# Kernel tuning notes

Hardware: AMD Instinct MI355X
Metric: run time of the kernel (lower is better)

Reference implementation:

```python
import jax, jax.numpy as jnp
import numpy as np

N_INNER = 2000  # number of inner tree nodes, divisible by 5 (gen_A grouping)
N_LEAF = 10000  # vocabulary / leaf count
N_DOC = 128     # number of documents


def _build_inv_A(n_inner):
    """Static structural matrix: A_full = I - [0 | A], inverted once (host-side numpy)."""
    m = n_inner // 5
    A = np.zeros((n_inner, n_inner - 1), dtype=np.float32)
    for r in range(m - 1):
        A[r, 5 * r:5 * r + 5] = 1.0
    A[m - 1, 5 * (m - 1):] = 1.0
    A_full = np.eye(n_inner, dtype=np.float32) - np.concatenate(
        [np.zeros((n_inner, 1), dtype=np.float32), A], axis=1)
    return jnp.asarray(np.linalg.inv(A_full))


def setup_inputs() -> dict:
    key = jax.random.key(0)
    k1, k2 = jax.random.split(key)
    mass = jax.random.uniform(k1, (N_DOC, N_LEAF), dtype=jnp.float32)
    mass = mass / mass.sum(axis=1, keepdims=True)  # probability mass per doc
    param = jax.random.normal(k2, (N_INNER, N_LEAF), dtype=jnp.float32)
    return {"mass": mass, "param": param}


def reference(mass, param):
    n_inner = param.shape[0]
    inv_A = _build_inv_A(n_inner)               # (n_inner, n_inner), static
    sm = jax.nn.softmax(param, axis=0)
    # hard column-wise argmax one-hot, as in calc_psub (ge of column max)
    B = (sm >= sm.max(axis=0, keepdims=True)).astype(mass.dtype)
    psub = inv_A @ B                            # (n_inner, n_leaf) subtree indicator
    # distance[i,j] = |psub @ (m_i - m_j)|_1 + |m_i - m_j|_1
    # = pairwise L1 on concatenated features [mass @ psub.T, mass]
    proj = mass @ psub.T                        # (n_doc, n_inner)
    feat = jnp.concatenate([proj, mass], axis=1)  # (n_doc, n_inner + n_leaf)
    return jnp.abs(feat[:, None, :] - feat[None, :, :]).sum(-1)  # (n_doc, n_doc)
```

## Files before the change

### kernel.cpp

```cpp
#include <hip/hip_runtime.h>

#define N_INNER 2000
#define N_LEAF  10000
#define N_DOC   128
#define AM_CHUNKS 50
#define AM_ROWS   40
#define DW   64
#define DCH  188

__global__ __launch_bounds__(256) void k_amax_part(const float* __restrict__ param,
                                                   float* __restrict__ pmax,
                                                   unsigned* __restrict__ pidx) {
    int j0 = (blockIdx.x * 256 + threadIdx.x) * 4;
    if (j0 >= N_LEAF) return;
    int r0 = blockIdx.y * AM_ROWS;
    float b0 = -1e30f, b1 = -1e30f, b2 = -1e30f, b3 = -1e30f;
    unsigned i0 = 0, i1 = 0, i2 = 0, i3 = 0;
    const float* p = param + (size_t)r0 * N_LEAF + j0;
    #pragma unroll 8
    for (int r = 0; r < AM_ROWS; ++r) {
        float4 v = *(const float4*)p;
        p += N_LEAF;
        unsigned row = (unsigned)(r0 + r);
        if (v.x > b0) { b0 = v.x; i0 = row; }
        if (v.y > b1) { b1 = v.y; i1 = row; }
        if (v.z > b2) { b2 = v.z; i2 = row; }
        if (v.w > b3) { b3 = v.w; i3 = row; }
    }
    size_t o = (size_t)blockIdx.y * N_LEAF + j0;
    *(float4*)(pmax + o) = make_float4(b0, b1, b2, b3);
    *(uint4*)(pidx + o)  = make_uint4(i0, i1, i2, i3);
}

__global__ __launch_bounds__(256) void k_amax_reduce(const float* __restrict__ pmax,
                                                     const unsigned* __restrict__ pidx,
                                                     int* __restrict__ amax) {
    int j = blockIdx.x * 256 + threadIdx.x;
    if (j >= N_LEAF) return;
    float best = pmax[j];
    unsigned bi = pidx[j];
    #pragma unroll 7
    for (int c = 1; c < AM_CHUNKS; ++c) {
        float v = pmax[(size_t)c * N_LEAF + j];
        if (v > best) { best = v; bi = pidx[(size_t)c * N_LEAF + j]; }
    }
    amax[j] = (int)bi;
}

__global__ __launch_bounds__(256) void k_wscan(const int* __restrict__ amax,
                                               const float* __restrict__ mass,
                                               float* __restrict__ Pex,
                                               float* __restrict__ S) {
    __shared__ float wl[N_INNER];
    __shared__ float sm[256];
    __shared__ float sm2[256];
    int d = blockIdx.x, t = threadIdx.x;
    for (int k = t; k < N_INNER; k += 256) wl[k] = 0.f;
    __syncthreads();
    const float* md = mass + (size_t)d * N_LEAF;
    for (int j = t; j < N_LEAF; j += 256) atomicAdd(&wl[amax[j]], md[j]);
    __syncthreads();
    float loc[8];
    float s = 0.f, s2 = 0.f;
    #pragma unroll
    for (int k = 0; k < 8; ++k) {
        int idx = t * 8 + k;
        float v = (idx < N_INNER) ? wl[idx] : 0.f;
        loc[k] = s;
        s += v;
        float dep = (float)((idx >= 1) + (idx >= 6) + (idx >= 31) + (idx >= 156) + (idx >= 781) + 2);
        s2 += dep * v;
    }
    sm[t] = s; sm2[t] = s2;
    __syncthreads();
    for (int off = 1; off < 256; off <<= 1) {
        float v = (t >= off) ? sm[t - off] : 0.f;
        __syncthreads();
        sm[t] += v;
        __syncthreads();
    }
    float base = sm[t] - s;
    float* Pd = Pex + (size_t)d * (N_INNER + 1);
    #pragma unroll
    for (int k = 0; k < 8; ++k) {
        int idx = t * 8 + k;
        if (idx <= N_INNER) Pd[idx] = base + loc[k];
    }
    for (int off = 128; off > 0; off >>= 1) {
        if (t < off) sm2[t] += sm2[t + off];
        __syncthreads();
    }
    if (t == 0) S[d] = sm2[0];
}

__global__ __launch_bounds__(256) void k_proj(const float* __restrict__ Pex,
                                              float* __restrict__ proj) {
    int id = blockIdx.x * 256 + threadIdx.x;
    int d = id / N_INNER;
    int i = id - d * N_INNER;
    const float* Pd = Pex + (size_t)d * (N_INNER + 1);
    float sum = 0.f;
    int s = i, e = i;
    while (s < N_INNER) {
        int ee = (e < N_INNER - 1) ? e : (N_INNER - 1);
        sum += Pd[ee + 1] - Pd[s];
        s = 5 * s + 1;
        e = 5 * e + 5;
    }
    proj[(size_t)d * N_INNER + i] = sum;
}

__global__ __launch_bounds__(256) void k_dist(const float* __restrict__ proj,
                                              const float* __restrict__ mass,
                                              float* __restrict__ partial) {
    __shared__ float lds[192 * DW];
    int t = threadIdx.x;
    int ch = blockIdx.x, jt = blockIdx.y;
    int c0 = ch * DW;
    int jbase = jt * 64;
    #pragma unroll
    for (int k = 0; k < 12; ++k) {
        int f = t + k * 256;
        int row = f >> 4, g = f & 15;
        int doc = (row < 128) ? row : (jbase + (row - 128));
        int col = c0 + g * 4;
        float4 v = make_float4(0.f, 0.f, 0.f, 0.f);
        if (col < N_INNER)            v = *(const float4*)(proj + (size_t)doc * N_INNER + col);
        else if (col < N_INNER + N_LEAF) v = *(const float4*)(mass + (size_t)doc * N_LEAF + (col - N_INNER));
        int gg = g ^ ((row >> 3) & 7);
        *(float4*)(&lds[row * DW + gg * 4]) = v;
    }
    __syncthreads();
    int tx = t & 15, ty = t >> 4;
    int ib = ty * 8;
    int jb = 128 + tx * 4;
    int swi = ty & 7;
    int swj = (tx >> 1) & 7;
    float acc[8][4];
    #pragma unroll
    for (int r = 0; r < 8; ++r)
        #pragma unroll
        for (int q = 0; q < 4; ++q) acc[r][q] = 0.f;
    #pragma unroll 4
    for (int cg = 0; cg < 16; ++cg) {
        float4 bv[4];
        #pragma unroll
        for (int jr = 0; jr < 4; ++jr)
            bv[jr] = *(const float4*)(&lds[(jb + jr) * DW + ((cg ^ swj) << 2)]);
        #pragma unroll
        for (int r = 0; r < 8; ++r) {
            float4 av = *(const float4*)(&lds[(ib + r) * DW + ((cg ^ swi) << 2)]);
            #pragma unroll
            for (int q = 0; q < 4; ++q) {
                acc[r][q] += (fminf(av.x, bv[q].x) + fminf(av.y, bv[q].y))
                           + (fminf(av.z, bv[q].z) + fminf(av.w, bv[q].w));
            }
        }
    }
    float* pp = partial + (size_t)ch * 16384 + jbase;
    #pragma unroll
    for (int r = 0; r < 8; ++r) {
        *(float4*)(pp + (size_t)(ib + r) * 128 + tx * 4) =
            make_float4(acc[r][0], acc[r][1], acc[r][2], acc[r][3]);
    }
}

__global__ __launch_bounds__(256) void k_out(const float* __restrict__ partial,
                                             const float* __restrict__ S,
                                             float* __restrict__ out) {
    int p = blockIdx.x * 256 + threadIdx.x;
    float s0 = 0.f, s1 = 0.f, s2 = 0.f, s3 = 0.f;
    #pragma unroll 8
    for (int c = 0; c < DCH; c += 4) {
        s0 += partial[(size_t)(c + 0) * 16384 + p];
        s1 += partial[(size_t)(c + 1) * 16384 + p];
        s2 += partial[(size_t)(c + 2) * 16384 + p];
        s3 += partial[(size_t)(c + 3) * 16384 + p];
    }
    int i = p >> 7, j = p & 127;
    out[p] = S[i] + S[j] - 2.f * ((s0 + s1) + (s2 + s3));
}

extern "C" void kernel_launch(void* const* d_in, const int* in_sizes, int n_in,
                              void* d_out, int out_size, void* d_ws, size_t ws_size,
                              hipStream_t stream) {
    const float* mass  = (const float*)d_in[0];
    const float* param = (const float*)d_in[1];
    float* out = (float*)d_out;
    char* ws = (char*)d_ws;

    float*    pmax    = (float*)(ws + 0);
    unsigned* pidx    = (unsigned*)(ws + 2000000);
    int*      amax    = (int*)(ws + 4000000);
    float*    Pex     = (float*)(ws + 4040000);
    float*    proj    = (float*)(ws + 5064512);
    float*    S       = (float*)(ws + 6088512);
    float*    partial = (float*)(ws + 6089024);

    k_amax_part  <<<dim3(10, AM_CHUNKS), 256, 0, stream>>>(param, pmax, pidx);
    k_amax_reduce<<<dim3(40),            256, 0, stream>>>(pmax, pidx, amax);
    k_wscan      <<<dim3(N_DOC),         256, 0, stream>>>(amax, mass, Pex, S);
    k_proj       <<<dim3(1000),          256, 0, stream>>>(Pex, proj);
    k_dist       <<<dim3(DCH, 2),        256, 0, stream>>>(proj, mass, partial);
    k_out        <<<dim3(64),            256, 0, stream>>>(partial, S, out);
}
```

Before: 190.4 us.

## Fuse argmax reduction via packed atomicMax and merge scan with projection

```diff
diff --git a/kernel.cpp b/kernel.cpp
--- a/kernel.cpp
+++ b/kernel.cpp
@@ -8,9 +8,13 @@
 #define DW   64
 #define DCH  188
 
-__global__ __launch_bounds__(256) void k_amax_part(const float* __restrict__ param,
-                                                   float* __restrict__ pmax,
-                                                   unsigned* __restrict__ pidx) {
+__device__ __forceinline__ unsigned enc_f32(float f) {
+    unsigned u = __float_as_uint(f);
+    return (u & 0x80000000u) ? ~u : (u | 0x80000000u);
+}
+
+__global__ __launch_bounds__(256) void k_amax(const float* __restrict__ param,
+                                              unsigned long long* __restrict__ packed) {
     int j0 = (blockIdx.x * 256 + threadIdx.x) * 4;
     if (j0 >= N_LEAF) return;
     int r0 = blockIdx.y * AM_ROWS;
@@ -27,38 +31,35 @@
         if (v.z > b2) { b2 = v.z; i2 = row; }
         if (v.w > b3) { b3 = v.w; i3 = row; }
     }
-    size_t o = (size_t)blockIdx.y * N_LEAF + j0;
-    *(float4*)(pmax + o) = make_float4(b0, b1, b2, b3);
-    *(uint4*)(pidx + o)  = make_uint4(i0, i1, i2, i3);
-}
-
-__global__ __launch_bounds__(256) void k_amax_reduce(const float* __restrict__ pmax,
-                                                     const unsigned* __restrict__ pidx,
-                                                     int* __restrict__ amax) {
-    int j = blockIdx.x * 256 + threadIdx.x;
-    if (j >= N_LEAF) return;
-    float best = pmax[j];
-    unsigned bi = pidx[j];
-    #pragma unroll 7
-    for (int c = 1; c < AM_CHUNKS; ++c) {
-        float v = pmax[(size_t)c * N_LEAF + j];
-        if (v > best) { best = v; bi = pidx[(size_t)c * N_LEAF + j]; }
-    }
-    amax[j] = (int)bi;
-}
-
-__global__ __launch_bounds__(256) void k_wscan(const int* __restrict__ amax,
-                                               const float* __restrict__ mass,
-                                               float* __restrict__ Pex,
-                                               float* __restrict__ S) {
+    atomicMax(&packed[j0 + 0], ((unsigned long long)enc_f32(b0) << 32) | i0);
+    atomicMax(&packed[j0 + 1], ((unsigned long long)enc_f32(b1) << 32) | i1);
+    atomicMax(&packed[j0 + 2], ((unsigned long long)enc_f32(b2) << 32) | i2);
+    atomicMax(&packed[j0 + 3], ((unsigned long long)enc_f32(b3) << 32) | i3);
+}
+
+__global__ __launch_bounds__(256) void k_wscan_proj(const unsigned long long* __restrict__ packed,
+                                                    const float* __restrict__ mass,
+                                                    float* __restrict__ proj,
+                                                    float* __restrict__ S) {
     __shared__ float wl[N_INNER];
-    __shared__ float sm[256];
-    __shared__ float sm2[256];
+    __shared__ float Px[N_INNER + 1];
+    __shared__ float wsum[4], wsum2[4];
     int d = blockIdx.x, t = threadIdx.x;
     for (int k = t; k < N_INNER; k += 256) wl[k] = 0.f;
     __syncthreads();
     const float* md = mass + (size_t)d * N_LEAF;
-    for (int j = t; j < N_LEAF; j += 256) atomicAdd(&wl[amax[j]], md[j]);
+    const unsigned* pw = (const unsigned*)packed;
+    #pragma unroll
+    for (int it = 0; it < 10; ++it) {
+        int j0 = (t + it * 256) * 4;
+        if (j0 < N_LEAF) {
+            float4 v = *(const float4*)(md + j0);
+            atomicAdd(&wl[pw[2 * (j0 + 0)]], v.x);
+            atomicAdd(&wl[pw[2 * (j0 + 1)]], v.y);
+            atomicAdd(&wl[pw[2 * (j0 + 2)]], v.z);
+            atomicAdd(&wl[pw[2 * (j0 + 3)]], v.w);
+        }
+    }
     __syncthreads();
     float loc[8];
     float s = 0.f, s2 = 0.f;
@@ -71,43 +72,44 @@
         float dep = (float)((idx >= 1) + (idx >= 6) + (idx >= 31) + (idx >= 156) + (idx >= 781) + 2);
         s2 += dep * v;
     }
-    sm[t] = s; sm2[t] = s2;
-    __syncthreads();
-    for (int off = 1; off < 256; off <<= 1) {
-        float v = (t >= off) ? sm[t - off] : 0.f;
-        __syncthreads();
-        sm[t] += v;
-        __syncthreads();
-    }
-    float base = sm[t] - s;
-    float* Pd = Pex + (size_t)d * (N_INNER + 1);
+    int lane = t & 63, w = t >> 6;
+    float ws = s;
+    #pragma unroll
+    for (int off = 1; off < 64; off <<= 1) {
+        float o = __shfl_up(ws, off, 64);
+        if (lane >= off) ws += o;
+    }
+    float r2 = s2;
+    #pragma unroll
+    for (int off = 32; off > 0; off >>= 1) r2 += __shfl_down(r2, off, 64);
+    if (lane == 63) wsum[w] = ws;
+    if (lane == 0)  wsum2[w] = r2;
+    __syncthreads();
+    float base = ws - s;
+    for (int q = 0; q < w; ++q) base += wsum[q];
     #pragma unroll
     for (int k = 0; k < 8; ++k) {
         int idx = t * 8 + k;
-        if (idx <= N_INNER) Pd[idx] = base + loc[k];
-    }
-    for (int off = 128; off > 0; off >>= 1) {
-        if (t < off) sm2[t] += sm2[t + off];
-        __syncthreads();
-    }
-    if (t == 0) S[d] = sm2[0];
-}
-
-__global__ __launch_bounds__(256) void k_proj(const float* __restrict__ Pex,
-                                              float* __restrict__ proj) {
-    int id = blockIdx.x * 256 + threadIdx.x;
-    int d = id / N_INNER;
-    int i = id - d * N_INNER;
-    const float* Pd = Pex + (size_t)d * (N_INNER + 1);
-    float sum = 0.f;
-    int s = i, e = i;
-    while (s < N_INNER) {
-        int ee = (e < N_INNER - 1) ? e : (N_INNER - 1);
-        sum += Pd[ee + 1] - Pd[s];
-        s = 5 * s + 1;
-        e = 5 * e + 5;
-    }
-    proj[(size_t)d * N_INNER + i] = sum;
+        if (idx <= N_INNER) Px[idx] = base + loc[k];
+    }
+    if (t == 0) S[d] = (wsum2[0] + wsum2[1]) + (wsum2[2] + wsum2[3]);
+    __syncthreads();
+    float* pd = proj + (size_t)d * N_INNER;
+    #pragma unroll
+    for (int k = 0; k < 8; ++k) {
+        int i = t + k * 256;
+        if (i < N_INNER) {
+            float sum = 0.f;
+            int s0 = i, e0 = i;
+            while (s0 < N_INNER) {
+                int ee = (e0 < N_INNER - 1) ? e0 : (N_INNER - 1);
+                sum += Px[ee + 1] - Px[s0];
+                s0 = 5 * s0 + 1;
+                e0 = 5 * e0 + 5;
+            }
+            pd[i] = sum;
+        }
+    }
 }
 
 __global__ __launch_bounds__(256) void k_dist(const float* __restrict__ proj,
@@ -125,7 +127,7 @@
         int doc = (row < 128) ? row : (jbase + (row - 128));
         int col = c0 + g * 4;
         float4 v = make_float4(0.f, 0.f, 0.f, 0.f);
-        if (col < N_INNER)            v = *(const float4*)(proj + (size_t)doc * N_INNER + col);
+        if (col < N_INNER)               v = *(const float4*)(proj + (size_t)doc * N_INNER + col);
         else if (col < N_INNER + N_LEAF) v = *(const float4*)(mass + (size_t)doc * N_LEAF + (col - N_INNER));
         int gg = g ^ ((row >> 3) & 7);
         *(float4*)(&lds[row * DW + gg * 4]) = v;
@@ -189,18 +191,14 @@
     float* out = (float*)d_out;
     char* ws = (char*)d_ws;
 
-    float*    pmax    = (float*)(ws + 0);
-    unsigned* pidx    = (unsigned*)(ws + 2000000);
-    int*      amax    = (int*)(ws + 4000000);
-    float*    Pex     = (float*)(ws + 4040000);
-    float*    proj    = (float*)(ws + 5064512);
-    float*    S       = (float*)(ws + 6088512);
-    float*    partial = (float*)(ws + 6089024);
-
-    k_amax_part  <<<dim3(10, AM_CHUNKS), 256, 0, stream>>>(param, pmax, pidx);
-    k_amax_reduce<<<dim3(40),            256, 0, stream>>>(pmax, pidx, amax);
-    k_wscan      <<<dim3(N_DOC),         256, 0, stream>>>(amax, mass, Pex, S);
-    k_proj       <<<dim3(1000),          256, 0, stream>>>(Pex, proj);
+    unsigned long long* packed = (unsigned long long*)(ws + 0);
+    float* proj    = (float*)(ws + 80000);
+    float* S       = (float*)(ws + 1104000);
+    float* partial = (float*)(ws + 1104512);
+
+    hipMemsetAsync(packed, 0, N_LEAF * sizeof(unsigned long long), stream);
+    k_amax       <<<dim3(10, AM_CHUNKS), 256, 0, stream>>>(param, packed);
+    k_wscan_proj <<<dim3(N_DOC),         256, 0, stream>>>(packed, mass, proj, S);
     k_dist       <<<dim3(DCH, 2),        256, 0, stream>>>(proj, mass, partial);
     k_out        <<<dim3(64),            256, 0, stream>>>(partial, S, out);
 }
```

Result: faster. 175.4 us (-7.9%).
